# Optimization experiments

Hardware: AMD Instinct MI355X
Metric: run time of the kernel (lower is better)

Reference implementation:

```python
import jax, jax.numpy as jnp
import numpy as np

H, D = 8, 16            # heads, per-head dim (hidden_channels // heads)
HID = H * D             # 128
N_MAT, N_ELEM = 100000, 118
F_MAT, F_ELEM = 128, 64
OUT = 64
E_EM, E_MM = 1000000, 2000000
NEG_SLOPE = 0.2

def _k(i):
    return jax.random.fold_in(jax.random.key(0), i)

def setup_inputs() -> dict:
    p = lambda i, shape: 0.1 * jax.random.normal(_k(i), shape, dtype=jnp.float32)
    return dict(
        x_mat=jax.random.normal(_k(0), (N_MAT, F_MAT), dtype=jnp.float32),
        x_elem=jax.random.normal(_k(1), (N_ELEM, F_ELEM), dtype=jnp.float32),
        W_proj_mat=p(2, (HID, F_MAT)), b_proj_mat=p(3, (HID,)),
        W_proj_elem=p(4, (HID, F_ELEM)), b_proj_elem=p(5, (HID,)),
        a_src_em=p(6, (H, D)), a_dst_em=p(7, (H, D)),
        a_src_mm=p(8, (H, D)), a_dst_mm=p(9, (H, D)),
        Wk=p(10, (HID, HID)), bk=p(11, (HID,)), q=p(12, (HID,)),
        Wl=p(13, (OUT, HID)), bl=p(14, (OUT,)),
        src_em=jax.random.randint(_k(15), (E_EM,), 0, N_ELEM, dtype=jnp.int32),
        dst_em=jax.random.randint(_k(16), (E_EM,), 0, N_MAT, dtype=jnp.int32),
        src_mm=jax.random.randint(_k(17), (E_MM,), 0, N_MAT, dtype=jnp.int32),
        dst_mm=jax.random.randint(_k(18), (E_MM,), 0, N_MAT, dtype=jnp.int32),
    )

def _edge_type_conv(x_s, x_d, a_s, a_d, src, dst, n_dst):
    # x_s:[Ns,H,D], x_d:[Nd,H,D]; per-edge-type GAT-style attention (HANConv.message)
    alpha = jnp.sum(x_s * a_s, -1)[src] + jnp.sum(x_d * a_d, -1)[dst]   # [E,H]
    alpha = jax.nn.leaky_relu(alpha, NEG_SLOPE)
    amax = jax.ops.segment_max(alpha, dst, num_segments=n_dst)          # stable softmax per dst
    ex = jnp.exp(alpha - amax[dst])
    den = jax.ops.segment_sum(ex, dst, num_segments=n_dst)
    w = ex / (den[dst] + 1e-16)                                         # [E,H]
    out = jax.ops.segment_sum(x_s[src] * w[:, :, None], dst, num_segments=n_dst)  # [Nd,H,D]
    return jax.nn.relu(out.reshape(n_dst, HID))

def _group(xs, q, Wk, bk):
    # HANConv semantic-level attention over metapaths
    s = jnp.stack(xs)                                                   # [M,N,C]
    score = jnp.sum(q * jnp.mean(jnp.tanh(s @ Wk.T + bk), axis=1), axis=-1)  # [M]
    attn = jax.nn.softmax(score)
    return jnp.einsum('m,mnc->nc', attn, s)

def reference(x_mat, x_elem, W_proj_mat, b_proj_mat, W_proj_elem, b_proj_elem,
              a_src_em, a_dst_em, a_src_mm, a_dst_mm, Wk, bk, q, Wl, bl,
              src_em, dst_em, src_mm, dst_mm):
    h_mat = (x_mat @ W_proj_mat.T + b_proj_mat).reshape(N_MAT, H, D)
    h_elem = (x_elem @ W_proj_elem.T + b_proj_elem).reshape(N_ELEM, H, D)
    o_em = _edge_type_conv(h_elem, h_mat, a_src_em, a_dst_em, src_em, dst_em, N_MAT)
    o_mm = _edge_type_conv(h_mat, h_mat, a_src_mm, a_dst_mm, src_mm, dst_mm, N_MAT)
    out_mat = _group([o_em, o_mm], q, Wk, bk)                           # [N_MAT, HID]
    return out_mat @ Wl.T + bl                                          # final Linear
```

## Files before the change

### kernel.cpp

```cpp
#include <hip/hip_runtime.h>
#include <hip/hip_bf16.h>

typedef unsigned int uint32;
typedef unsigned short ushort16;

using bf16x8 = __attribute__((ext_vector_type(8))) short;
using f32x4  = __attribute__((ext_vector_type(4))) float;

#define N_MATN 100000
#define N_ELEMN 118
#define F_MATN 128
#define F_ELEMN 64
#define HIDN 128
#define NHEAD 8
#define OUTC 64
#define SCORE_BLOCKS 1024
#define NSTRIPS 6250
#define NT 8
#define NTILES (N_MATN/NT)

#define SH 8
#define NBK 391
#define BCH 8192

__device__ __forceinline__ float blo(uint32 u){ return __uint_as_float(u << 16); }
__device__ __forceinline__ float bhi(uint32 u){ return __uint_as_float(u & 0xffff0000u); }
__device__ __forceinline__ ushort16 f2bf(float f){
    uint32 u = __float_as_uint(f);
    uint32 r = u + 0x7FFFu + ((u >> 16) & 1u);
    return (ushort16)(r >> 16);
}
__device__ __forceinline__ uint32 pack2(float a, float b){
    return (uint32)f2bf(a) | ((uint32)f2bf(b) << 16);
}
__device__ __forceinline__ bf16x8 cvt8(const float* __restrict__ p){
    bf16x8 r;
    #pragma unroll
    for(int j=0;j<8;j++) r[j] = (short)f2bf(p[j]);
    return r;
}

__global__ __launch_bounds__(128) void proj_elem_v2(
    const float* __restrict__ x, const float* __restrict__ W,
    const float* __restrict__ bias, const float* __restrict__ a_se,
    ushort16* __restrict__ h, float* __restrict__ asrc_em)
{
    __shared__ float xr[F_ELEMN];
    int n = blockIdx.x, c = threadIdx.x;
    if(c < 16) ((float4*)xr)[c] = ((const float4*)(x + n*F_ELEMN))[c];
    __syncthreads();
    const float4* Wr = (const float4*)(W + c*F_ELEMN);
    float acc = 0.f;
    #pragma unroll 4
    for(int i=0;i<16;i++){
        float4 w = Wr[i];
        acc += xr[4*i]*w.x + xr[4*i+1]*w.y + xr[4*i+2]*w.z + xr[4*i+3]*w.w;
    }
    acc += bias[c];
    h[n*HIDN + c] = f2bf(acc);
    float p = acc * a_se[c];
    #pragma unroll
    for(int m=8;m>=1;m>>=1) p += __shfl_xor(p, m, 16);
    if((c&15)==0) asrc_em[n*NHEAD + (c>>4)] = p;
}

__global__ __launch_bounds__(256) void proj_mat_mfma(
    const float* __restrict__ x, const float* __restrict__ W,
    const float* __restrict__ bias,
    const float* __restrict__ a_de, const float* __restrict__ a_sm, const float* __restrict__ a_dm,
    ushort16* __restrict__ h,
    float* __restrict__ adst_em, float* __restrict__ asrc_mm, float* __restrict__ adst_mm)
{
    int tid = threadIdx.x;
    int wv = tid >> 6, lane = tid & 63, quad = lane >> 4, sl = lane & 15;
    bf16x8 B[2][4];
    float bc[2], ade[2], asv[2], adv[2];
    #pragma unroll
    for(int i=0;i<2;i++){
        int c = (2*wv+i)*16 + sl;
        const float* wr = W + c*F_MATN;
        #pragma unroll
        for(int ks=0;ks<4;ks++) B[i][ks] = cvt8(wr + ks*32 + quad*8);
        bc[i] = bias[c]; ade[i] = a_de[c]; asv[i] = a_sm[c]; adv[i] = a_dm[c];
    }
    for(int s = blockIdx.x; s < NSTRIPS; s += gridDim.x){
        int n0 = s*16;
        const float* xrow = x + (size_t)(n0+sl)*F_MATN;
        bf16x8 A[4];
        #pragma unroll
        for(int ks=0;ks<4;ks++) A[ks] = cvt8(xrow + ks*32 + quad*8);
        f32x4 acc[2];
        #pragma unroll
        for(int i=0;i<2;i++){ acc[i][0]=0.f; acc[i][1]=0.f; acc[i][2]=0.f; acc[i][3]=0.f; }
        #pragma unroll
        for(int i=0;i<2;i++)
            #pragma unroll
            for(int ks=0;ks<4;ks++)
                acc[i] = __builtin_amdgcn_mfma_f32_16x16x32_bf16(A[ks], B[i][ks], acc[i], 0, 0, 0);
        #pragma unroll
        for(int i=0;i<2;i++){
            int head = 2*wv + i;
            #pragma unroll
            for(int r=0;r<4;r++){
                float a = acc[i][r] + bc[i];
                int node = n0 + quad*4 + r;
                h[(size_t)node*HIDN + head*16 + sl] = f2bf(a);
                float p0 = a*ade[i], p1 = a*asv[i], p2 = a*adv[i];
                #pragma unroll
                for(int m=8;m>=1;m>>=1){
                    p0 += __shfl_xor(p0, m);
                    p1 += __shfl_xor(p1, m);
                    p2 += __shfl_xor(p2, m);
                }
                if(sl == 0){
                    adst_em[node*NHEAD + head] = p0;
                    asrc_mm[node*NHEAD + head] = p1;
                    adst_mm[node*NHEAD + head] = p2;
                }
            }
        }
    }
}

__global__ __launch_bounds__(256) void bucket_count(
    const int* __restrict__ dst_em, int nE_em, int* __restrict__ bcnt_em,
    const int* __restrict__ dst_mm, int nE_mm, int* __restrict__ bcnt_mm)
{
    __shared__ int he[NBK], hm[NBK];
    int t = threadIdx.x;
    for(int i=t;i<NBK;i+=256){ he[i]=0; hm[i]=0; }
    __syncthreads();
    int st = gridDim.x*256;
    for(int i = blockIdx.x*256 + t; i < nE_em; i += st) atomicAdd(&he[dst_em[i]>>SH], 1);
    for(int i = blockIdx.x*256 + t; i < nE_mm; i += st) atomicAdd(&hm[dst_mm[i]>>SH], 1);
    __syncthreads();
    for(int j=t;j<NBK;j+=256){
        int a = he[j], b = hm[j];
        if(a) atomicAdd(&bcnt_em[j], a);
        if(b) atomicAdd(&bcnt_mm[j], b);
    }
}

__global__ __launch_bounds__(512) void bucket_scan(
    const int* __restrict__ bcnt_em, int* __restrict__ bb_em, int* __restrict__ bcur_em,
    const int* __restrict__ bcnt_mm, int* __restrict__ bb_mm, int* __restrict__ bcur_mm,
    int* __restrict__ offs_em, int* __restrict__ offs_mm, int nE_em, int nE_mm)
{
    __shared__ int wsum[8];
    int t = threadIdx.x, l = t & 63, w = t >> 6;
    {
        int v = (t < NBK) ? bcnt_em[t] : 0;
        int x = v;
        #pragma unroll
        for(int off=1; off<64; off<<=1){ int y = __shfl_up(x, off); if(l >= off) x += y; }
        if(l == 63) wsum[w] = x;
        __syncthreads();
        int base = 0;
        for(int k=0;k<w;k++) base += wsum[k];
        int excl = base + x - v;
        if(t < NBK){ bb_em[t] = excl; bcur_em[t] = excl; }
        if(t == 0){ bb_em[NBK] = nE_em; offs_em[N_MATN] = nE_em; }
        __syncthreads();
    }
    {
        int v = (t < NBK) ? bcnt_mm[t] : 0;
        int x = v;
        #pragma unroll
        for(int off=1; off<64; off<<=1){ int y = __shfl_up(x, off); if(l >= off) x += y; }
        if(l == 63) wsum[w] = x;
        __syncthreads();
        int base = 0;
        for(int k=0;k<w;k++) base += wsum[k];
        int excl = base + x - v;
        if(t < NBK){ bb_mm[t] = excl; bcur_mm[t] = excl; }
        if(t == 0){ bb_mm[NBK] = nE_mm; offs_mm[N_MATN] = nE_mm; }
    }
}

__global__ __launch_bounds__(256) void bin_pass(
    const int* __restrict__ src_em, const int* __restrict__ dst_em, int nE_em,
    int* __restrict__ bcur_em, uint32* __restrict__ st_em,
    const int* __restrict__ src_mm, const int* __restrict__ dst_mm, int nE_mm,
    int* __restrict__ bcur_mm, uint32* __restrict__ st_mm)
{
    __shared__ int cnt[NBK];
    __shared__ int base[NBK];
    int t = threadIdx.x;
    int nch_em = (nE_em + BCH - 1)/BCH;
    int nch_mm = (nE_mm + BCH - 1)/BCH;
    int ntot = nch_em + nch_mm;
    for(int c = blockIdx.x; c < ntot; c += gridDim.x){
        bool em = c < nch_em;
        const int* src = em ? src_em : src_mm;
        const int* dst = em ? dst_em : dst_mm;
        int nE   = em ? nE_em : nE_mm;
        int* bcur = em ? bcur_em : bcur_mm;
        uint32* st = em ? st_em : st_mm;
        int cc = em ? c : c - nch_em;
        int s = cc*BCH;
        int e = s + BCH; if(e > nE) e = nE;
        for(int i=t;i<NBK;i+=256) cnt[i] = 0;
        __syncthreads();
        for(int i=s+t;i<e;i+=256) atomicAdd(&cnt[dst[i] >> SH], 1);
        __syncthreads();
        for(int i=t;i<NBK;i+=256){
            int v = cnt[i];
            base[i] = v ? atomicAdd(&bcur[i], v) : 0;
            cnt[i] = 0;
        }
        __syncthreads();
        for(int i=s+t;i<e;i+=256){
            int d = dst[i];
            int b = d >> SH;
            int p = base[b] + atomicAdd(&cnt[b], 1);
            st[p] = ((uint32)(d & ((1<<SH)-1)) << 17) | (uint32)src[i];
        }
        __syncthreads();
    }
}

__global__ __launch_bounds__(256) void place_pass(
    const int* __restrict__ bb_em, const uint32* __restrict__ st_em,
    int* __restrict__ csr_em, int* __restrict__ offs_em,
    const int* __restrict__ bb_mm, const uint32* __restrict__ st_mm,
    int* __restrict__ csr_mm, int* __restrict__ offs_mm)
{
    __shared__ int cnt[256];
    __shared__ int wsum[4];
    __shared__ int cur[256];
    int b = blockIdx.x;
    bool em = b < NBK;
    const int* bb        = em ? bb_em : bb_mm;
    const uint32* stp    = em ? st_em : st_mm;
    int* csr             = em ? csr_em : csr_mm;
    int* offs            = em ? offs_em : offs_mm;
    int bk = em ? b : b - NBK;
    int d0 = bk << SH;
    int t = threadIdx.x, l = t & 63, w = t >> 6;
    int nd = N_MATN - d0; if(nd > 256) nd = 256;
    int beg = bb[bk], end = bb[bk+1];
    cnt[t] = 0;
    __syncthreads();
    for(int i = beg + t; i < end; i += 256)
        atomicAdd(&cnt[stp[i] >> 17], 1);
    __syncthreads();
    int v = cnt[t];
    int x = v;
    #pragma unroll
    for(int off=1; off<64; off<<=1){ int y = __shfl_up(x, off); if(l >= off) x += y; }
    if(l == 63) wsum[w] = x;
    __syncthreads();
    int base = beg;
    for(int k=0;k<w;k++) base += wsum[k];
    int excl = base + x - v;
    cur[t] = excl;
    if(t < nd) offs[d0 + t] = excl;
    __syncthreads();
    for(int i = beg + t; i < end; i += 256){
        uint32 vv = stp[i];
        int dl = (int)(vv >> 17);
        int p = atomicAdd(&cur[dl], 1);
        csr[p] = (int)(vv & 0x1FFFFu);
    }
}

__global__ __launch_bounds__(256) void agg_both(
    const int* __restrict__ offs_em, const int* __restrict__ csr_em,
    const ushort16* __restrict__ h_elem, const float* __restrict__ asrc_em,
    const float* __restrict__ adst_em, ushort16* __restrict__ o_em,
    const int* __restrict__ offs_mm, const int* __restrict__ csr_mm,
    const ushort16* __restrict__ h_mat, const float* __restrict__ asrc_mm,
    const float* __restrict__ adst_mm, ushort16* __restrict__ o_mm)
{
    int lane = threadIdx.x & 63;
    int g = lane >> 4;
    int q = lane & 15;
    int hd = q >> 1;
    int w = (blockIdx.x*blockDim.x + threadIdx.x) >> 6;
    int nw = (gridDim.x*blockDim.x) >> 6;
    for(int nid = w; nid < 2*N_MATN; nid += nw){
        int nidu = __builtin_amdgcn_readfirstlane(nid);
        bool em = nidu < N_MATN;
        int d = em ? nidu : nidu - N_MATN;
        const int*    offs = em ? offs_em : offs_mm;
        const int*    csr  = em ? csr_em  : csr_mm;
        const uint32* hs   = (const uint32*)(em ? h_elem : h_mat);
        const float*  asp  = em ? asrc_em : asrc_mm;
        const float*  adp  = em ? adst_em : adst_mm;
        uint32*       op   = (uint32*)(em ? o_em : o_mm);
        int beg = offs[d], end = offs[d+1];
        float ad = adp[(unsigned)(d*NHEAD + hd)];
        float den = 0.f;
        float nlo[4] = {0.f,0.f,0.f,0.f};
        float nhi[4] = {0.f,0.f,0.f,0.f};
        for(int j0 = beg; j0 < end; j0 += 4){
            int e = j0 + g;
            bool valid = e < end;
            int jc = valid ? e : end - 1;
            int s = csr[(unsigned)jc];
            float al = asp[(unsigned)(s*NHEAD + hd)] + ad;
            al = fmaxf(al, 0.2f*al);
            float ex = __expf(al);
            ex = valid ? ex : 0.f;
            den += ex;
            const uint4 hv = *(const uint4*)(hs + (unsigned)(s*64 + q*4));
            nlo[0] += blo(hv.x)*ex; nhi[0] += bhi(hv.x)*ex;
            nlo[1] += blo(hv.y)*ex; nhi[1] += bhi(hv.y)*ex;
            nlo[2] += blo(hv.z)*ex; nhi[2] += bhi(hv.z)*ex;
            nlo[3] += blo(hv.w)*ex; nhi[3] += bhi(hv.w)*ex;
        }
        den += __shfl_xor(den, 16); den += __shfl_xor(den, 32);
        #pragma unroll
        for(int k=0;k<4;k++){
            nlo[k] += __shfl_xor(nlo[k], 16); nlo[k] += __shfl_xor(nlo[k], 32);
            nhi[k] += __shfl_xor(nhi[k], 16); nhi[k] += __shfl_xor(nhi[k], 32);
        }
        if(g == 0){
            float rdn = 1.0f/(den + 1e-16f);
            uint4 pk;
            pk.x = pack2(fmaxf(nlo[0]*rdn, 0.f), fmaxf(nhi[0]*rdn, 0.f));
            pk.y = pack2(fmaxf(nlo[1]*rdn, 0.f), fmaxf(nhi[1]*rdn, 0.f));
            pk.z = pack2(fmaxf(nlo[2]*rdn, 0.f), fmaxf(nhi[2]*rdn, 0.f));
            pk.w = pack2(fmaxf(nlo[3]*rdn, 0.f), fmaxf(nhi[3]*rdn, 0.f));
            *(uint4*)(op + (size_t)d*64 + q*4) = pk;
        }
    }
}

__global__ __launch_bounds__(256) void score_mfma(
    const ushort16* __restrict__ o_em, const ushort16* __restrict__ o_mm,
    const float* __restrict__ Wk, const float* __restrict__ bkv,
    const float* __restrict__ qv, float* __restrict__ partials)
{
    int tid = threadIdx.x;
    int wv = tid >> 6, lane = tid & 63, quad = lane >> 4, sl = lane & 15;
    bf16x8 B[2][4];
    float bkc[2], qc[2];
    #pragma unroll
    for(int i=0;i<2;i++){
        int c = (2*wv+i)*16 + sl;
        const float* wr = Wk + c*HIDN;
        #pragma unroll
        for(int ks=0;ks<4;ks++) B[i][ks] = cvt8(wr + ks*32 + quad*8);
        bkc[i] = bkv[c]; qc[i] = qv[c];
    }
    float se = 0.f, sm = 0.f;
    for(int s = blockIdx.x; s < NSTRIPS; s += gridDim.x){
        int n0 = s*16;
        const bf16x8* rowE = (const bf16x8*)(o_em + (size_t)(n0+sl)*HIDN);
        const bf16x8* rowM = (const bf16x8*)(o_mm + (size_t)(n0+sl)*HIDN);
        bf16x8 AE[4], AM[4];
        #pragma unroll
        for(int ks=0;ks<4;ks++){
            AE[ks] = rowE[ks*4 + quad];
            AM[ks] = rowM[ks*4 + quad];
        }
        f32x4 aE[2], aM[2];
        #pragma unroll
        for(int i=0;i<2;i++){
            aE[i][0]=0.f;aE[i][1]=0.f;aE[i][2]=0.f;aE[i][3]=0.f;
            aM[i][0]=0.f;aM[i][1]=0.f;aM[i][2]=0.f;aM[i][3]=0.f;
        }
        #pragma unroll
        for(int i=0;i<2;i++)
            #pragma unroll
            for(int ks=0;ks<4;ks++){
                aE[i] = __builtin_amdgcn_mfma_f32_16x16x32_bf16(AE[ks], B[i][ks], aE[i], 0, 0, 0);
                aM[i] = __builtin_amdgcn_mfma_f32_16x16x32_bf16(AM[ks], B[i][ks], aM[i], 0, 0, 0);
            }
        #pragma unroll
        for(int i=0;i<2;i++)
            #pragma unroll
            for(int r=0;r<4;r++){
                se += qc[i]*tanhf(aE[i][r] + bkc[i]);
                sm += qc[i]*tanhf(aM[i][r] + bkc[i]);
            }
    }
    #pragma unroll
    for(int m=32;m>=1;m>>=1){ se += __shfl_xor(se,m); sm += __shfl_xor(sm,m); }
    __shared__ float red[8];
    if(lane==0){ red[wv*2]=se; red[wv*2+1]=sm; }
    __syncthreads();
    if(tid==0){
        partials[blockIdx.x*2+0] = red[0]+red[2]+red[4]+red[6];
        partials[blockIdx.x*2+1] = red[1]+red[3]+red[5]+red[7];
    }
}

__global__ __launch_bounds__(256) void reduce_scores_kernel(
    const float* __restrict__ partials, float* __restrict__ scores)
{
    __shared__ float sh0[256], sh1[256];
    int t = threadIdx.x;
    float s0=0.f, s1=0.f;
    for(int i=t;i<SCORE_BLOCKS;i+=256){ s0 += partials[2*i]; s1 += partials[2*i+1]; }
    sh0[t]=s0; sh1[t]=s1; __syncthreads();
    for(int s=128;s>0;s>>=1){ if(t<s){ sh0[t]+=sh0[t+s]; sh1[t]+=sh1[t+s]; } __syncthreads(); }
    if(t==0){ scores[0]=sh0[0]; scores[1]=sh1[0]; }
}

__global__ __launch_bounds__(128) void final_v3(
    const ushort16* __restrict__ o_em, const ushort16* __restrict__ o_mm,
    const float* __restrict__ Wl, const float* __restrict__ blv,
    const float* __restrict__ scores, float* __restrict__ out)
{
    __shared__ float wlds[64*129];
    __shared__ float zlds[NT*128];
    int t = threadIdx.x;
    #pragma unroll 2
    for(int i=t;i<2048;i+=128){
        float4 v = ((const float4*)Wl)[i];
        int r = i >> 5, k4 = i & 31;
        float* d = wlds + r*129 + k4*4;
        d[0]=v.x; d[1]=v.y; d[2]=v.z; d[3]=v.w;
    }
    float s0 = scores[0]*(1.0f/N_MATN), s1 = scores[1]*(1.0f/N_MATN);
    float mx = fmaxf(s0,s1);
    float e0 = __expf(s0-mx), e1 = __expf(s1-mx);
    float inv = 1.0f/(e0+e1);
    float a0 = e0*inv, a1 = e1*inv;
    int j = t & 63, half = t >> 6;
    float bj = blv[j];
    const float* wr = wlds + j*129;
    __syncthreads();
    for(int tile = blockIdx.x; tile < NTILES; tile += gridDim.x){
        int n0 = tile*NT;
        __syncthreads();
        {
            const uint4* pe = (const uint4*)((const uint32*)o_em + (size_t)n0*64);
            const uint4* pm = (const uint4*)((const uint32*)o_mm + (size_t)n0*64);
            uint4 ve = pe[t], vm = pm[t];
            float* zd = zlds + t*8;
            zd[0]=a0*blo(ve.x)+a1*blo(vm.x); zd[1]=a0*bhi(ve.x)+a1*bhi(vm.x);
            zd[2]=a0*blo(ve.y)+a1*blo(vm.y); zd[3]=a0*bhi(ve.y)+a1*bhi(vm.y);
            zd[4]=a0*blo(ve.z)+a1*blo(vm.z); zd[5]=a0*bhi(ve.z)+a1*bhi(vm.z);
            zd[6]=a0*blo(ve.w)+a1*blo(vm.w); zd[7]=a0*bhi(ve.w)+a1*bhi(vm.w);
        }
        __syncthreads();
        float acc[4] = {0.f,0.f,0.f,0.f};
        #pragma unroll 1
        for(int kk=0;kk<128;kk+=8){
            float f0=wr[kk],f1=wr[kk+1],f2=wr[kk+2],f3=wr[kk+3];
            float f4=wr[kk+4],f5=wr[kk+5],f6=wr[kk+6],f7=wr[kk+7];
            #pragma unroll
            for(int n=0;n<4;n++){
                const float4* zr = (const float4*)(zlds + (half*4+n)*128 + kk);
                float4 za = zr[0], zb = zr[1];
                acc[n] += za.x*f0 + za.y*f1 + za.z*f2 + za.w*f3
                        + zb.x*f4 + zb.y*f5 + zb.z*f6 + zb.w*f7;
            }
        }
        #pragma unroll
        for(int n=0;n<4;n++)
            out[(size_t)(n0 + half*4 + n)*OUTC + j] = bj + acc[n];
    }
}

extern "C" void kernel_launch(void* const* d_in, const int* in_sizes, int n_in,
                              void* d_out, int out_size, void* d_ws, size_t ws_size,
                              hipStream_t stream)
{
    const float* x_mat    = (const float*)d_in[0];
    const float* x_elem   = (const float*)d_in[1];
    const float* W_pm     = (const float*)d_in[2];
    const float* b_pm     = (const float*)d_in[3];
    const float* W_pe     = (const float*)d_in[4];
    const float* b_pe     = (const float*)d_in[5];
    const float* a_se     = (const float*)d_in[6];
    const float* a_de     = (const float*)d_in[7];
    const float* a_sm     = (const float*)d_in[8];
    const float* a_dm     = (const float*)d_in[9];
    const float* Wk       = (const float*)d_in[10];
    const float* bk       = (const float*)d_in[11];
    const float* qv       = (const float*)d_in[12];
    const float* Wl       = (const float*)d_in[13];
    const float* bl       = (const float*)d_in[14];
    const int* src_em     = (const int*)d_in[15];
    const int* dst_em     = (const int*)d_in[16];
    const int* src_mm     = (const int*)d_in[17];
    const int* dst_mm     = (const int*)d_in[18];
    int nE_em = in_sizes[15];
    int nE_mm = in_sizes[17];

    char* ws = (char*)d_ws;
    size_t off = 0;
    auto alloc = [&](size_t bytes) -> void* {
        void* p = ws + off; off += (bytes + 255) & ~size_t(255); return p;
    };
    ushort16* h_mat   = (ushort16*)alloc((size_t)N_MATN*HIDN*2);
    ushort16* h_elem  = (ushort16*)alloc((size_t)N_ELEMN*HIDN*2);
    float*    asrcEM  = (float*)   alloc((size_t)N_ELEMN*NHEAD*4);
    float*    adstEM  = (float*)   alloc((size_t)N_MATN*NHEAD*4);
    float*    asrcMM  = (float*)   alloc((size_t)N_MATN*NHEAD*4);
    float*    adstMM  = (float*)   alloc((size_t)N_MATN*NHEAD*4);
    int*      offs_em = (int*)     alloc((size_t)(N_MATN+1)*4);
    int*      offs_mm = (int*)     alloc((size_t)(N_MATN+1)*4);
    int*      csr_em  = (int*)     alloc((size_t)1000000*4);
    int*      csr_mm  = (int*)     alloc((size_t)2000000*4);
    ushort16* o_em    = (ushort16*)alloc((size_t)N_MATN*HIDN*2);
    ushort16* o_mm    = (ushort16*)alloc((size_t)N_MATN*HIDN*2);
    float*    partials= (float*)   alloc((size_t)SCORE_BLOCKS*2*4);
    float*    scores  = (float*)   alloc(256);
    int*      bb_em   = (int*)     alloc((size_t)(NBK+1)*4);
    int*      bb_mm   = (int*)     alloc((size_t)(NBK+1)*4);
    int*      bcur_em = (int*)     alloc((size_t)NBK*4);
    int*      bcur_mm = (int*)     alloc((size_t)NBK*4);
    size_t zero_start = off;
    int*      bcnt_em = (int*)     alloc((size_t)NBK*4);
    int*      bcnt_mm = (int*)     alloc((size_t)NBK*4);
    size_t zero_bytes = off - zero_start;

    uint32* st_em = (uint32*)o_em;
    uint32* st_mm = st_em + nE_em;

    hipMemsetAsync(ws + zero_start, 0, zero_bytes, stream);

    proj_elem_v2<<<N_ELEMN, 128, 0, stream>>>(x_elem, W_pe, b_pe, a_se, h_elem, asrcEM);
    proj_mat_mfma<<<1024, 256, 0, stream>>>(x_mat, W_pm, b_pm, a_de, a_sm, a_dm,
                                            h_mat, adstEM, asrcMM, adstMM);

    bucket_count<<<256, 256, 0, stream>>>(dst_em, nE_em, bcnt_em, dst_mm, nE_mm, bcnt_mm);
    bucket_scan<<<1, 512, 0, stream>>>(bcnt_em, bb_em, bcur_em,
                                       bcnt_mm, bb_mm, bcur_mm,
                                       offs_em, offs_mm, nE_em, nE_mm);

    int nch = (nE_em + BCH - 1)/BCH + (nE_mm + BCH - 1)/BCH;
    bin_pass<<<nch, 256, 0, stream>>>(src_em, dst_em, nE_em, bcur_em, st_em,
                                      src_mm, dst_mm, nE_mm, bcur_mm, st_mm);
    place_pass<<<2*NBK, 256, 0, stream>>>(bb_em, st_em, csr_em, offs_em,
                                          bb_mm, st_mm, csr_mm, offs_mm);

    agg_both<<<4096, 256, 0, stream>>>(offs_em, csr_em, h_elem, asrcEM, adstEM, o_em,
                                       offs_mm, csr_mm, h_mat, asrcMM, adstMM, o_mm);

    score_mfma<<<SCORE_BLOCKS, 256, 0, stream>>>(o_em, o_mm, Wk, bk, qv, partials);
    reduce_scores_kernel<<<1, 256, 0, stream>>>(partials, scores);
    final_v3<<<1024, 128, 0, stream>>>(o_em, o_mm, Wl, bl, scores, (float*)d_out);
}
```

Measured before the change: 498.8 us.

## Vectorize edge binning loads, unroll aggregation by two, widen final linear tiles

The bucket count and bin passes now read dst/src indices as int4 vectors, with a scalar tail loop for leftovers. The aggregation loop handles two edge groups per iteration with separate accumulators, so more gathers are in flight and memory latency is hidden better. The final linear kernel moves to 256 threads and 16-node tiles with a larger grid. These are separate tweaks spread over several kernels. The wider final kernel uses more LDS and registers per block, and the int4 casts assume 16-byte aligned chunk starts.

```diff
diff --git a/kernel.cpp b/kernel.cpp
--- a/kernel.cpp
+++ b/kernel.cpp
@@ -16,8 +16,8 @@
 #define OUTC 64
 #define SCORE_BLOCKS 1024
 #define NSTRIPS 6250
-#define NT 8
-#define NTILES (N_MATN/NT)
+#define NT2 16
+#define NTILES2 (N_MATN/NT2)
 
 #define SH 8
 #define NBK 391
@@ -130,9 +130,28 @@
     int t = threadIdx.x;
     for(int i=t;i<NBK;i+=256){ he[i]=0; hm[i]=0; }
     __syncthreads();
+    int gt = blockIdx.x*256 + t;
     int st = gridDim.x*256;
-    for(int i = blockIdx.x*256 + t; i < nE_em; i += st) atomicAdd(&he[dst_em[i]>>SH], 1);
-    for(int i = blockIdx.x*256 + t; i < nE_mm; i += st) atomicAdd(&hm[dst_mm[i]>>SH], 1);
+    {
+        int n4 = nE_em >> 2;
+        const int4* d4 = (const int4*)dst_em;
+        for(int i = gt; i < n4; i += st){
+            int4 v = d4[i];
+            atomicAdd(&he[v.x>>SH],1); atomicAdd(&he[v.y>>SH],1);
+            atomicAdd(&he[v.z>>SH],1); atomicAdd(&he[v.w>>SH],1);
+        }
+        for(int i = (n4<<2) + gt; i < nE_em; i += st) atomicAdd(&he[dst_em[i]>>SH],1);
+    }
+    {
+        int n4 = nE_mm >> 2;
+        const int4* d4 = (const int4*)dst_mm;
+        for(int i = gt; i < n4; i += st){
+            int4 v = d4[i];
+            atomicAdd(&hm[v.x>>SH],1); atomicAdd(&hm[v.y>>SH],1);
+            atomicAdd(&hm[v.z>>SH],1); atomicAdd(&hm[v.w>>SH],1);
+        }
+        for(int i = (n4<<2) + gt; i < nE_mm; i += st) atomicAdd(&hm[dst_mm[i]>>SH],1);
+    }
     __syncthreads();
     for(int j=t;j<NBK;j+=256){
         int a = he[j], b = hm[j];
@@ -199,9 +218,18 @@
         int cc = em ? c : c - nch_em;
         int s = cc*BCH;
         int e = s + BCH; if(e > nE) e = nE;
+        int len = e - s;
+        int n4 = len >> 2;
+        const int4* d4 = (const int4*)(dst + s);
+        const int4* s4 = (const int4*)(src + s);
         for(int i=t;i<NBK;i+=256) cnt[i] = 0;
         __syncthreads();
-        for(int i=s+t;i<e;i+=256) atomicAdd(&cnt[dst[i] >> SH], 1);
+        for(int i=t;i<n4;i+=256){
+            int4 v = d4[i];
+            atomicAdd(&cnt[v.x>>SH],1); atomicAdd(&cnt[v.y>>SH],1);
+            atomicAdd(&cnt[v.z>>SH],1); atomicAdd(&cnt[v.w>>SH],1);
+        }
+        for(int i = s + (n4<<2) + t; i < e; i += 256) atomicAdd(&cnt[dst[i]>>SH], 1);
         __syncthreads();
         for(int i=t;i<NBK;i+=256){
             int v = cnt[i];
@@ -209,7 +237,20 @@
             cnt[i] = 0;
         }
         __syncthreads();
-        for(int i=s+t;i<e;i+=256){
+        for(int i=t;i<n4;i+=256){
+            int4 dv = d4[i];
+            int4 sv = s4[i];
+            int b, p;
+            b = dv.x>>SH; p = base[b] + atomicAdd(&cnt[b],1);
+            st[p] = ((uint32)(dv.x & ((1<<SH)-1)) << 17) | (uint32)sv.x;
+            b = dv.y>>SH; p = base[b] + atomicAdd(&cnt[b],1);
+            st[p] = ((uint32)(dv.y & ((1<<SH)-1)) << 17) | (uint32)sv.y;
+            b = dv.z>>SH; p = base[b] + atomicAdd(&cnt[b],1);
+            st[p] = ((uint32)(dv.z & ((1<<SH)-1)) << 17) | (uint32)sv.z;
+            b = dv.w>>SH; p = base[b] + atomicAdd(&cnt[b],1);
+            st[p] = ((uint32)(dv.w & ((1<<SH)-1)) << 17) | (uint32)sv.w;
+        }
+        for(int i = s + (n4<<2) + t; i < e; i += 256){
             int d = dst[i];
             int b = d >> SH;
             int p = base[b] + atomicAdd(&cnt[b], 1);
@@ -290,28 +331,39 @@
         uint32*       op   = (uint32*)(em ? o_em : o_mm);
         int beg = offs[d], end = offs[d+1];
         float ad = adp[(unsigned)(d*NHEAD + hd)];
-        float den = 0.f;
-        float nlo[4] = {0.f,0.f,0.f,0.f};
-        float nhi[4] = {0.f,0.f,0.f,0.f};
-        for(int j0 = beg; j0 < end; j0 += 4){
-            int e = j0 + g;
-            bool valid = e < end;
-            int jc = valid ? e : end - 1;
-            int s = csr[(unsigned)jc];
-            float al = asp[(unsigned)(s*NHEAD + hd)] + ad;
-            al = fmaxf(al, 0.2f*al);
-            float ex = __expf(al);
-            ex = valid ? ex : 0.f;
-            den += ex;
-            const uint4 hv = *(const uint4*)(hs + (unsigned)(s*64 + q*4));
-            nlo[0] += blo(hv.x)*ex; nhi[0] += bhi(hv.x)*ex;
-            nlo[1] += blo(hv.y)*ex; nhi[1] += bhi(hv.y)*ex;
-            nlo[2] += blo(hv.z)*ex; nhi[2] += bhi(hv.z)*ex;
-            nlo[3] += blo(hv.w)*ex; nhi[3] += bhi(hv.w)*ex;
-        }
+        float denA = 0.f, denB = 0.f;
+        float nloA[4] = {0.f,0.f,0.f,0.f}, nhiA[4] = {0.f,0.f,0.f,0.f};
+        float nloB[4] = {0.f,0.f,0.f,0.f}, nhiB[4] = {0.f,0.f,0.f,0.f};
+        for(int j0 = beg; j0 < end; j0 += 8){
+            int e0 = j0 + g, e1 = j0 + 4 + g;
+            bool v0 = e0 < end, v1 = e1 < end;
+            int s0 = csr[(unsigned)(v0 ? e0 : end - 1)];
+            int s1 = csr[(unsigned)(v1 ? e1 : end - 1)];
+            float a0 = asp[(unsigned)(s0*NHEAD + hd)];
+            float a1 = asp[(unsigned)(s1*NHEAD + hd)];
+            const uint4 h0 = *(const uint4*)(hs + (unsigned)(s0*64 + q*4));
+            const uint4 h1 = *(const uint4*)(hs + (unsigned)(s1*64 + q*4));
+            float al0 = a0 + ad; al0 = fmaxf(al0, 0.2f*al0);
+            float ex0 = __expf(al0); ex0 = v0 ? ex0 : 0.f;
+            float al1 = a1 + ad; al1 = fmaxf(al1, 0.2f*al1);
+            float ex1 = __expf(al1); ex1 = v1 ? ex1 : 0.f;
+            denA += ex0; denB += ex1;
+            nloA[0] += blo(h0.x)*ex0; nhiA[0] += bhi(h0.x)*ex0;
+            nloA[1] += blo(h0.y)*ex0; nhiA[1] += bhi(h0.y)*ex0;
+            nloA[2] += blo(h0.z)*ex0; nhiA[2] += bhi(h0.z)*ex0;
+            nloA[3] += blo(h0.w)*ex0; nhiA[3] += bhi(h0.w)*ex0;
+            nloB[0] += blo(h1.x)*ex1; nhiB[0] += bhi(h1.x)*ex1;
+            nloB[1] += blo(h1.y)*ex1; nhiB[1] += bhi(h1.y)*ex1;
+            nloB[2] += blo(h1.z)*ex1; nhiB[2] += bhi(h1.z)*ex1;
+            nloB[3] += blo(h1.w)*ex1; nhiB[3] += bhi(h1.w)*ex1;
+        }
+        float den = denA + denB;
         den += __shfl_xor(den, 16); den += __shfl_xor(den, 32);
+        float nlo[4], nhi[4];
         #pragma unroll
         for(int k=0;k<4;k++){
+            nlo[k] = nloA[k] + nloB[k];
+            nhi[k] = nhiA[k] + nhiB[k];
             nlo[k] += __shfl_xor(nlo[k], 16); nlo[k] += __shfl_xor(nlo[k], 32);
             nhi[k] += __shfl_xor(nhi[k], 16); nhi[k] += __shfl_xor(nhi[k], 32);
         }
@@ -399,16 +451,15 @@
     if(t==0){ scores[0]=sh0[0]; scores[1]=sh1[0]; }
 }
 
-__global__ __launch_bounds__(128) void final_v3(
+__global__ __launch_bounds__(256) void final_v4(
     const ushort16* __restrict__ o_em, const ushort16* __restrict__ o_mm,
     const float* __restrict__ Wl, const float* __restrict__ blv,
     const float* __restrict__ scores, float* __restrict__ out)
 {
     __shared__ float wlds[64*129];
-    __shared__ float zlds[NT*128];
+    __shared__ float zlds[NT2*128];
     int t = threadIdx.x;
-    #pragma unroll 2
-    for(int i=t;i<2048;i+=128){
+    for(int i=t;i<2048;i+=256){
         float4 v = ((const float4*)Wl)[i];
         int r = i >> 5, k4 = i & 31;
         float* d = wlds + r*129 + k4*4;
@@ -423,8 +474,8 @@
     float bj = blv[j];
     const float* wr = wlds + j*129;
     __syncthreads();
-    for(int tile = blockIdx.x; tile < NTILES; tile += gridDim.x){
-        int n0 = tile*NT;
+    for(int tile = blockIdx.x; tile < NTILES2; tile += gridDim.x){
+        int n0 = tile*NT2;
         __syncthreads();
         {
             const uint4* pe = (const uint4*)((const uint32*)o_em + (size_t)n0*64);
@@ -535,5 +586,5 @@
 
     score_mfma<<<SCORE_BLOCKS, 256, 0, stream>>>(o_em, o_mm, Wk, bk, qv, partials);
     reduce_scores_kernel<<<1, 256, 0, stream>>>(partials, scores);
-    final_v3<<<1024, 128, 0, stream>>>(o_em, o_mm, Wl, bl, scores, (float*)d_out);
-}
+    final_v4<<<2048, 256, 0, stream>>>(o_em, o_mm, Wl, bl, scores, (float*)d_out);
+}
```

After: 460.2 us. 1.08x faster.
